# Kernel optimization log

Measured on AMD Instinct MI355X. Metric: run time of the kernel, lower is better.

The kernel has to match this reference:

```python
import jax, jax.numpy as jnp
import numpy as np

TEMP = 1.0

def setup_inputs() -> dict:
    key = jax.random.key(0)
    k1, k2, k3 = jax.random.split(key, 3)
    B, Lq, Lk, X, Dv = 16, 1024, 1024, 512, 512
    h_q = jax.random.normal(k1, (B, Lq, X), dtype=jnp.float32)
    h_k = jax.random.normal(k2, (B, Lk, X), dtype=jnp.float32)
    h_v = jax.random.normal(k3, (B, Lk, Dv), dtype=jnp.float32)
    return {"h_q": h_q, "h_k": h_k, "h_v": h_v}

def reference(h_q, h_k, h_v):
    # Original computes full cross-batch 'abx,cdx->acbd' then extracts the
    # batch diagonal; that equals a direct per-batch QK^T: [B,Lq,Lk].
    atten_score = jnp.einsum('bqx,bkx->bqk', h_q, h_k) / TEMP
    atten_prob = jax.nn.softmax(atten_score, axis=-1)  # dropout is identity in eval
    cxt = jnp.einsum('bqk,bkd->bqd', atten_prob, h_v)
    return cxt
```

## Files before the change

kernel.cpp:

```cpp
#include <hip/hip_runtime.h>

typedef _Float16 half8 __attribute__((ext_vector_type(8)));
typedef float f32x4 __attribute__((ext_vector_type(4)));
typedef unsigned short u16x8 __attribute__((ext_vector_type(8)));

#define LOG2E 1.44269504088896340736f

constexpr int NB = 16, LQ = 1024, LK = 1024, DX = 512, DVD = 512;
constexpr int QBLK = 64, KVB = 32, NCH = LK / KVB;
constexpr int TILE = KVB * DX;

static __device__ __forceinline__ unsigned short f2h(float f) {
  union { _Float16 h; unsigned short u; } c; c.h = (_Float16)f; return c.u;
}
static __device__ __forceinline__ unsigned int pack2(float a, float b) {
  union { _Float16 h[2]; unsigned int u; } c;
  c.h[0] = (_Float16)a; c.h[1] = (_Float16)b; return c.u;
}
static __device__ __forceinline__ void gload16(const unsigned short* g, unsigned short* l) {
  __builtin_amdgcn_global_load_lds(
      (const __attribute__((address_space(1))) unsigned int*)g,
      (__attribute__((address_space(3))) unsigned int*)l, 16, 0, 0);
}

__global__ __launch_bounds__(256) void prep_kv(
    const float* __restrict__ K, const float* __restrict__ V,
    unsigned short* __restrict__ Kw, unsigned short* __restrict__ Vw) {
  __shared__ float tile[32][520];
  const int bidx = blockIdx.x;
  const bool isV = bidx >= NB * NCH;
  const int bc = isV ? bidx - NB * NCH : bidx;
  const int t = (int)threadIdx.x;

  const float* src = (isV ? V : K) + (size_t)bc * (KVB * DX);
#pragma unroll
  for (int i = 0; i < 16; ++i) {
    int idx = t + i * 256;
    int r = idx >> 7, cc = (idx & 127) * 4;
    float4 v = *(const float4*)(src + (size_t)idx * 4);
    *(float4*)&tile[r][cc] = v;
  }
  __syncthreads();

  unsigned short* dst = (isV ? Vw : Kw) + (size_t)bc * TILE;
  if (!isV) {
#pragma unroll
    for (int k = 0; k < 8; ++k) {
      int obi = t * 8 + k;
      int p = obi >> 5, kv = obi & 31;
      const float* rp = &tile[kv][p * 8];
      u16x8 o = { f2h(rp[0]), f2h(rp[1]), f2h(rp[2]), f2h(rp[3]),
                  f2h(rp[4]), f2h(rp[5]), f2h(rp[6]), f2h(rp[7]) };
      *(u16x8*)(dst + obi * 8) = o;
    }
  } else {
#pragma unroll
    for (int k = 0; k < 8; ++k) {
      int vbi = t * 8 + k;
      int pv = vbi >> 9, d = vbi & 511;
      u16x8 o = { f2h(tile[pv * 8 + 0][d]), f2h(tile[pv * 8 + 1][d]),
                  f2h(tile[pv * 8 + 2][d]), f2h(tile[pv * 8 + 3][d]),
                  f2h(tile[pv * 8 + 4][d]), f2h(tile[pv * 8 + 5][d]),
                  f2h(tile[pv * 8 + 6][d]), f2h(tile[pv * 8 + 7][d]) };
      *(u16x8*)(dst + vbi * 8) = o;
    }
  }
}

__global__ __launch_bounds__(768) void attn_ws(
    const float* __restrict__ Qf, const unsigned short* __restrict__ Kw,
    const unsigned short* __restrict__ Vw, float* __restrict__ Out) {
  __shared__ __align__(16) unsigned short Kl[2][TILE];
  __shared__ __align__(16) unsigned short Vl[2][TILE];
  __shared__ __align__(16) unsigned short Pl[2][2048];
  __shared__ __align__(16) float sml[2][64];
  __shared__ __align__(16) float lfin[64];
  __shared__ __align__(16) int rflag[2][4];

  const int bid = blockIdx.x;
  const int logical = (bid & 7) * 32 + (bid >> 3);
  const int b  = logical >> 4;
  const int qt = logical & 15;
  const int tid = (int)threadIdx.x;
  const int lane = tid & 63;
  const int wave = tid >> 6;
  const bool isQK = wave < 4;
  const int qs = wave;
  const int wd = wave - 4;
  const int c15 = lane & 15;
  const int g4  = lane >> 4;
  const int rbase = g4 * 4;

  f32x4 blk[16];
  float mr = -3.0e38f, lr = 0.f;

  if (isQK) {
    const float* qrow = Qf + ((size_t)b * LQ + qt * QBLK + qs * 16 + c15) * DX + g4 * 8;
#pragma unroll
    for (int ks = 0; ks < 16; ++ks) {
      float4 a0 = *(const float4*)(qrow + ks * 32);
      float4 a1 = *(const float4*)(qrow + ks * 32 + 4);
      half8 f;
      f[0] = (_Float16)(a0.x * LOG2E); f[1] = (_Float16)(a0.y * LOG2E);
      f[2] = (_Float16)(a0.z * LOG2E); f[3] = (_Float16)(a0.w * LOG2E);
      f[4] = (_Float16)(a1.x * LOG2E); f[5] = (_Float16)(a1.y * LOG2E);
      f[6] = (_Float16)(a1.z * LOG2E); f[7] = (_Float16)(a1.w * LOG2E);
      blk[ks] = __builtin_bit_cast(f32x4, f);
    }
  } else {
#pragma unroll
    for (int i = 0; i < 16; ++i) blk[i] = (f32x4){0.f, 0.f, 0.f, 0.f};
  }

  const int st = tid - 256;
  const unsigned short* kg = Kw + (size_t)b * NCH * TILE + st * 8;
  const unsigned short* vg = Vw + (size_t)b * NCH * TILE + st * 8;

  if (tid >= 256) {
#pragma unroll
    for (int ii = 0; ii < 4; ++ii) gload16(kg + ii * 4096, &Kl[0][st * 8 + ii * 4096]);
  }
  __syncthreads();

  for (int p = 0; p <= NCH; ++p) {
    const int cb = p & 1, pbuf = cb ^ 1;

    if (tid >= 256) {
      if (p + 1 < NCH) {
        const unsigned short* ks_ = kg + (size_t)(p + 1) * TILE;
#pragma unroll
        for (int ii = 0; ii < 4; ++ii)
          gload16(ks_ + ii * 4096, &Kl[pbuf][st * 8 + ii * 4096]);
      }
      if (p < NCH) {
        const unsigned short* vs_ = vg + (size_t)p * TILE;
#pragma unroll
        for (int ii = 0; ii < 4; ++ii)
          gload16(vs_ + ii * 4096, &Vl[cb][st * 8 + ii * 4096]);
      }
    }

    if (isQK) {
      if (p < NCH) {
        f32x4 cs0 = {0.f, 0.f, 0.f, 0.f};
        f32x4 cs1 = {0.f, 0.f, 0.f, 0.f};
        __builtin_amdgcn_s_setprio(1);
#pragma unroll
        for (int ks = 0; ks < 16; ++ks) {
          const int po = (ks * 4 + g4) * 256;
          half8 a0 = *(const half8*)&Kl[cb][c15 * 8 + po];
          half8 a1 = *(const half8*)&Kl[cb][(16 + c15) * 8 + po];
          half8 qv = __builtin_bit_cast(half8, blk[ks]);
          cs0 = __builtin_amdgcn_mfma_f32_16x16x32_f16(a0, qv, cs0, 0, 0, 0);
          cs1 = __builtin_amdgcn_mfma_f32_16x16x32_f16(a1, qv, cs1, 0, 0, 0);
        }
        __builtin_amdgcn_s_setprio(0);

        float pm = fmaxf(fmaxf(fmaxf(cs0[0], cs0[1]), fmaxf(cs0[2], cs0[3])),
                         fmaxf(fmaxf(cs1[0], cs1[1]), fmaxf(cs1[2], cs1[3])));
        pm = fmaxf(pm, __shfl_xor(pm, 16, 64));
        pm = fmaxf(pm, __shfl_xor(pm, 32, 64));
        const bool resc = __any(pm > mr + 8.0f);
        float scl = 1.0f;
        if (resc) {
          float mn = fmaxf(mr, pm);
          scl = exp2f(mr - mn);
          mr = mn;
        }
        if (g4 == 0) sml[cb][qs * 16 + c15] = scl;
        if (lane == 0) rflag[cb][qs] = resc ? 1 : 0;
        float p0[4], p1[4];
#pragma unroll
        for (int j = 0; j < 4; ++j) {
          p0[j] = exp2f(cs0[j] - mr);
          p1[j] = exp2f(cs1[j] - mr);
        }
        float ps = ((p0[0] + p0[1]) + (p0[2] + p0[3]))
                 + ((p1[0] + p1[1]) + (p1[2] + p1[3]));
        ps += __shfl_xor(ps, 16, 64);
        ps += __shfl_xor(ps, 32, 64);
        lr = lr * scl + ps;

        {
          unsigned short* pw = &Pl[cb][(g4 >> 1) * 512 + (qs * 16 + c15) * 8 + (g4 & 1) * 4];
          uint2 w0 = { pack2(p0[0], p0[1]), pack2(p0[2], p0[3]) };
          uint2 w1 = { pack2(p1[0], p1[1]), pack2(p1[2], p1[3]) };
          *(uint2*)pw          = w0;
          *(uint2*)(pw + 1024) = w1;
        }
        if (p == NCH - 1 && g4 == 0) lfin[qs * 16 + c15] = lr;
      }
    } else {
      if (p > 0) {
        int4 f4 = *(const int4*)&rflag[pbuf][0];
        const int fl = f4.x | f4.y | f4.z | f4.w;
        half8 pa0 = *(const half8*)&Pl[pbuf][g4 * 512 + (c15) * 8];
        half8 pa1 = *(const half8*)&Pl[pbuf][g4 * 512 + (16 + c15) * 8];
        half8 pa2 = *(const half8*)&Pl[pbuf][g4 * 512 + (32 + c15) * 8];
        half8 pa3 = *(const half8*)&Pl[pbuf][g4 * 512 + (48 + c15) * 8];
        half8 bv0 = *(const half8*)&Vl[pbuf][g4 * 4096 + (wd * 64 + c15) * 8];
        half8 bv1 = *(const half8*)&Vl[pbuf][g4 * 4096 + (wd * 64 + 16 + c15) * 8];
        half8 bv2 = *(const half8*)&Vl[pbuf][g4 * 4096 + (wd * 64 + 32 + c15) * 8];
        half8 bv3 = *(const half8*)&Vl[pbuf][g4 * 4096 + (wd * 64 + 48 + c15) * 8];
        if (fl) {
#pragma unroll
          for (int s = 0; s < 4; ++s) {
            f32x4 sv = *(const f32x4*)&sml[pbuf][s * 16 + rbase];
#pragma unroll
            for (int n = 0; n < 4; ++n)
#pragma unroll
              for (int j = 0; j < 4; ++j) blk[s * 4 + n][j] *= sv[j];
          }
        }
        __builtin_amdgcn_s_setprio(1);
#pragma unroll
        for (int s = 0; s < 4; ++s) {
          half8 pas = (s == 0) ? pa0 : (s == 1) ? pa1 : (s == 2) ? pa2 : pa3;
          blk[s * 4 + 0] = __builtin_amdgcn_mfma_f32_16x16x32_f16(pas, bv0, blk[s * 4 + 0], 0, 0, 0);
          blk[s * 4 + 1] = __builtin_amdgcn_mfma_f32_16x16x32_f16(pas, bv1, blk[s * 4 + 1], 0, 0, 0);
          blk[s * 4 + 2] = __builtin_amdgcn_mfma_f32_16x16x32_f16(pas, bv2, blk[s * 4 + 2], 0, 0, 0);
          blk[s * 4 + 3] = __builtin_amdgcn_mfma_f32_16x16x32_f16(pas, bv3, blk[s * 4 + 3], 0, 0, 0);
        }
        __builtin_amdgcn_s_setprio(0);
      }
    }

    asm volatile("s_waitcnt vmcnt(0) lgkmcnt(0)" ::: "memory");
    __builtin_amdgcn_s_barrier();
    __builtin_amdgcn_sched_barrier(0);
  }

  if (!isQK) {
#pragma unroll
    for (int s = 0; s < 4; ++s) {
      f32x4 lv = *(const f32x4*)&lfin[s * 16 + rbase];
      float inv[4];
#pragma unroll
      for (int j = 0; j < 4; ++j) inv[j] = 1.0f / lv[j];
      float* ob = Out + ((size_t)b * LQ + qt * QBLK + s * 16 + rbase) * DVD
                  + wd * 64 + c15;
#pragma unroll
      for (int n = 0; n < 4; ++n)
#pragma unroll
        for (int j = 0; j < 4; ++j)
          ob[(size_t)j * DVD + n * 16] = blk[s * 4 + n][j] * inv[j];
    }
  }
}

extern "C" void kernel_launch(void* const* d_in, const int* in_sizes, int n_in,
                              void* d_out, int out_size, void* d_ws, size_t ws_size,
                              hipStream_t stream) {
  const float* Qf = (const float*)d_in[0];
  const float* Kf = (const float*)d_in[1];
  const float* Vf = (const float*)d_in[2];
  float* Out = (float*)d_out;

  unsigned short* Kw = (unsigned short*)d_ws;
  unsigned short* Vw = Kw + (size_t)NB * NCH * TILE;

  prep_kv<<<NB * NCH * 2, 256, 0, stream>>>(Kf, Vf, Kw, Vw);
  attn_ws<<<NB * (LQ / QBLK), 768, 0, stream>>>(Qf, Kw, Vw, Out);
}
```

Baseline: 79.96 us.

## Double KV chunk size and read V directly from global instead of LDS

Raises the KV chunk from 32 to 64 keys, halving the number of barrier-synchronised phases, and adjusts the prep kernel to emit the wider packed layout. V is no longer staged in LDS; the PV waves load their V fragments straight from global/L2 into registers. Only K is double-buffered in LDS, and the loader waves now also issue those copies. This frees LDS and cuts synchronisation, at the cost of exposing global-load latency on the V path, more register pressure, and a launch_bounds occupancy hint.

```diff
diff --git a/kernel.cpp b/kernel.cpp
--- a/kernel.cpp
+++ b/kernel.cpp
@@ -7,7 +7,7 @@
 #define LOG2E 1.44269504088896340736f
 
 constexpr int NB = 16, LQ = 1024, LK = 1024, DX = 512, DVD = 512;
-constexpr int QBLK = 64, KVB = 32, NCH = LK / KVB;
+constexpr int QBLK = 64, KVB = 64, NCH = LK / KVB;
 constexpr int TILE = KVB * DX;
 
 static __device__ __forceinline__ unsigned short f2h(float f) {
@@ -28,51 +28,51 @@
     unsigned short* __restrict__ Kw, unsigned short* __restrict__ Vw) {
   __shared__ float tile[32][520];
   const int bidx = blockIdx.x;
-  const bool isV = bidx >= NB * NCH;
-  const int bc = isV ? bidx - NB * NCH : bidx;
+  const bool isV = bidx >= NB * NCH * 2;
+  const int r = isV ? bidx - NB * NCH * 2 : bidx;
+  const int b = r >> 5, sub = r & 31, c = sub >> 1, half = sub & 1;
   const int t = (int)threadIdx.x;
 
-  const float* src = (isV ? V : K) + (size_t)bc * (KVB * DX);
+  const float* src = (isV ? V : K) + ((size_t)b * LK + c * 64 + half * 32) * DX;
 #pragma unroll
   for (int i = 0; i < 16; ++i) {
     int idx = t + i * 256;
-    int r = idx >> 7, cc = (idx & 127) * 4;
+    int rr = idx >> 7, cc = (idx & 127) * 4;
     float4 v = *(const float4*)(src + (size_t)idx * 4);
-    *(float4*)&tile[r][cc] = v;
+    *(float4*)&tile[rr][cc] = v;
   }
   __syncthreads();
 
-  unsigned short* dst = (isV ? Vw : Kw) + (size_t)bc * TILE;
+  unsigned short* dst = (isV ? Vw : Kw) + (size_t)(b * NCH + c) * TILE;
   if (!isV) {
 #pragma unroll
     for (int k = 0; k < 8; ++k) {
       int obi = t * 8 + k;
-      int p = obi >> 5, kv = obi & 31;
-      const float* rp = &tile[kv][p * 8];
+      int p = obi >> 5, kvloc = obi & 31;
+      const float* rp = &tile[kvloc][p * 8];
       u16x8 o = { f2h(rp[0]), f2h(rp[1]), f2h(rp[2]), f2h(rp[3]),
                   f2h(rp[4]), f2h(rp[5]), f2h(rp[6]), f2h(rp[7]) };
-      *(u16x8*)(dst + obi * 8) = o;
+      *(u16x8*)(dst + p * 512 + (half * 32 + kvloc) * 8) = o;
     }
   } else {
 #pragma unroll
     for (int k = 0; k < 8; ++k) {
       int vbi = t * 8 + k;
-      int pv = vbi >> 9, d = vbi & 511;
-      u16x8 o = { f2h(tile[pv * 8 + 0][d]), f2h(tile[pv * 8 + 1][d]),
-                  f2h(tile[pv * 8 + 2][d]), f2h(tile[pv * 8 + 3][d]),
-                  f2h(tile[pv * 8 + 4][d]), f2h(tile[pv * 8 + 5][d]),
-                  f2h(tile[pv * 8 + 6][d]), f2h(tile[pv * 8 + 7][d]) };
-      *(u16x8*)(dst + vbi * 8) = o;
-    }
-  }
-}
-
-__global__ __launch_bounds__(768) void attn_ws(
+      int pvloc = vbi >> 9, d = vbi & 511;
+      u16x8 o = { f2h(tile[pvloc * 8 + 0][d]), f2h(tile[pvloc * 8 + 1][d]),
+                  f2h(tile[pvloc * 8 + 2][d]), f2h(tile[pvloc * 8 + 3][d]),
+                  f2h(tile[pvloc * 8 + 4][d]), f2h(tile[pvloc * 8 + 5][d]),
+                  f2h(tile[pvloc * 8 + 6][d]), f2h(tile[pvloc * 8 + 7][d]) };
+      *(u16x8*)(dst + (half * 4 + pvloc) * 4096 + d * 8) = o;
+    }
+  }
+}
+
+__global__ __launch_bounds__(768, 3) void attn_ws2(
     const float* __restrict__ Qf, const unsigned short* __restrict__ Kw,
     const unsigned short* __restrict__ Vw, float* __restrict__ Out) {
   __shared__ __align__(16) unsigned short Kl[2][TILE];
-  __shared__ __align__(16) unsigned short Vl[2][TILE];
-  __shared__ __align__(16) unsigned short Pl[2][2048];
+  __shared__ __align__(16) unsigned short Pl[2][8 * 64 * 8];
   __shared__ __align__(16) float sml[2][64];
   __shared__ __align__(16) float lfin[64];
   __shared__ __align__(16) int rflag[2][4];
@@ -90,10 +90,11 @@
   const int c15 = lane & 15;
   const int g4  = lane >> 4;
   const int rbase = g4 * 4;
-
-  f32x4 blk[16];
+  const int d0 = wd * 64;
+
+  half8 qfrag[16];
+  f32x4 acc[16];
   float mr = -3.0e38f, lr = 0.f;
-
   if (isQK) {
     const float* qrow = Qf + ((size_t)b * LQ + qt * QBLK + qs * 16 + c15) * DX + g4 * 8;
 #pragma unroll
@@ -105,59 +106,52 @@
       f[2] = (_Float16)(a0.z * LOG2E); f[3] = (_Float16)(a0.w * LOG2E);
       f[4] = (_Float16)(a1.x * LOG2E); f[5] = (_Float16)(a1.y * LOG2E);
       f[6] = (_Float16)(a1.z * LOG2E); f[7] = (_Float16)(a1.w * LOG2E);
-      blk[ks] = __builtin_bit_cast(f32x4, f);
+      qfrag[ks] = f;
     }
   } else {
 #pragma unroll
-    for (int i = 0; i < 16; ++i) blk[i] = (f32x4){0.f, 0.f, 0.f, 0.f};
+    for (int i = 0; i < 16; ++i) acc[i] = (f32x4){0.f, 0.f, 0.f, 0.f};
   }
 
   const int st = tid - 256;
   const unsigned short* kg = Kw + (size_t)b * NCH * TILE + st * 8;
-  const unsigned short* vg = Vw + (size_t)b * NCH * TILE + st * 8;
+  const unsigned short* vgb = Vw + (size_t)b * NCH * TILE;
 
   if (tid >= 256) {
 #pragma unroll
-    for (int ii = 0; ii < 4; ++ii) gload16(kg + ii * 4096, &Kl[0][st * 8 + ii * 4096]);
+    for (int ii = 0; ii < 8; ++ii) gload16(kg + ii * 4096, &Kl[0][st * 8 + ii * 4096]);
   }
   __syncthreads();
 
-  for (int p = 0; p <= NCH; ++p) {
-    const int cb = p & 1, pbuf = cb ^ 1;
-
-    if (tid >= 256) {
-      if (p + 1 < NCH) {
-        const unsigned short* ks_ = kg + (size_t)(p + 1) * TILE;
-#pragma unroll
-        for (int ii = 0; ii < 4; ++ii)
-          gload16(ks_ + ii * 4096, &Kl[pbuf][st * 8 + ii * 4096]);
-      }
-      if (p < NCH) {
-        const unsigned short* vs_ = vg + (size_t)p * TILE;
-#pragma unroll
-        for (int ii = 0; ii < 4; ++ii)
-          gload16(vs_ + ii * 4096, &Vl[cb][st * 8 + ii * 4096]);
-      }
-    }
+  for (int ph = 0; ph <= NCH; ++ph) {
+    const int cb = ph & 1, pb = cb ^ 1;
 
     if (isQK) {
-      if (p < NCH) {
-        f32x4 cs0 = {0.f, 0.f, 0.f, 0.f};
-        f32x4 cs1 = {0.f, 0.f, 0.f, 0.f};
-        __builtin_amdgcn_s_setprio(1);
-#pragma unroll
-        for (int ks = 0; ks < 16; ++ks) {
-          const int po = (ks * 4 + g4) * 256;
-          half8 a0 = *(const half8*)&Kl[cb][c15 * 8 + po];
-          half8 a1 = *(const half8*)&Kl[cb][(16 + c15) * 8 + po];
-          half8 qv = __builtin_bit_cast(half8, blk[ks]);
-          cs0 = __builtin_amdgcn_mfma_f32_16x16x32_f16(a0, qv, cs0, 0, 0, 0);
-          cs1 = __builtin_amdgcn_mfma_f32_16x16x32_f16(a1, qv, cs1, 0, 0, 0);
-        }
-        __builtin_amdgcn_s_setprio(0);
+      if (ph < NCH) {
+        f32x4 cs0 = {0.f,0.f,0.f,0.f}, cs1 = {0.f,0.f,0.f,0.f};
+        f32x4 cs2 = {0.f,0.f,0.f,0.f}, cs3 = {0.f,0.f,0.f,0.f};
+        {
+          const unsigned short* kb = &Kl[cb][c15 * 8];
+          __builtin_amdgcn_s_setprio(1);
+#pragma unroll
+          for (int ks = 0; ks < 16; ++ks) {
+            const int po = (ks * 4 + g4) * 512;
+            half8 a0 = *(const half8*)(kb + po);
+            half8 a1 = *(const half8*)(kb + po + 128);
+            half8 a2 = *(const half8*)(kb + po + 256);
+            half8 a3 = *(const half8*)(kb + po + 384);
+            cs0 = __builtin_amdgcn_mfma_f32_16x16x32_f16(a0, qfrag[ks], cs0, 0, 0, 0);
+            cs1 = __builtin_amdgcn_mfma_f32_16x16x32_f16(a1, qfrag[ks], cs1, 0, 0, 0);
+            cs2 = __builtin_amdgcn_mfma_f32_16x16x32_f16(a2, qfrag[ks], cs2, 0, 0, 0);
+            cs3 = __builtin_amdgcn_mfma_f32_16x16x32_f16(a3, qfrag[ks], cs3, 0, 0, 0);
+          }
+          __builtin_amdgcn_s_setprio(0);
+        }
 
         float pm = fmaxf(fmaxf(fmaxf(cs0[0], cs0[1]), fmaxf(cs0[2], cs0[3])),
                          fmaxf(fmaxf(cs1[0], cs1[1]), fmaxf(cs1[2], cs1[3])));
+        pm = fmaxf(pm, fmaxf(fmaxf(fmaxf(cs2[0], cs2[1]), fmaxf(cs2[2], cs2[3])),
+                             fmaxf(fmaxf(cs3[0], cs3[1]), fmaxf(cs3[2], cs3[3]))));
         pm = fmaxf(pm, __shfl_xor(pm, 16, 64));
         pm = fmaxf(pm, __shfl_xor(pm, 32, 64));
         const bool resc = __any(pm > mr + 8.0f);
@@ -169,58 +163,76 @@
         }
         if (g4 == 0) sml[cb][qs * 16 + c15] = scl;
         if (lane == 0) rflag[cb][qs] = resc ? 1 : 0;
-        float p0[4], p1[4];
+
+        float p0[4], p1[4], p2[4], p3[4];
 #pragma unroll
         for (int j = 0; j < 4; ++j) {
           p0[j] = exp2f(cs0[j] - mr);
           p1[j] = exp2f(cs1[j] - mr);
-        }
-        float ps = ((p0[0] + p0[1]) + (p0[2] + p0[3]))
-                 + ((p1[0] + p1[1]) + (p1[2] + p1[3]));
-        ps += __shfl_xor(ps, 16, 64);
-        ps += __shfl_xor(ps, 32, 64);
-        lr = lr * scl + ps;
-
+          p2[j] = exp2f(cs2[j] - mr);
+          p3[j] = exp2f(cs3[j] - mr);
+        }
         {
           unsigned short* pw = &Pl[cb][(g4 >> 1) * 512 + (qs * 16 + c15) * 8 + (g4 & 1) * 4];
           uint2 w0 = { pack2(p0[0], p0[1]), pack2(p0[2], p0[3]) };
           uint2 w1 = { pack2(p1[0], p1[1]), pack2(p1[2], p1[3]) };
+          uint2 w2 = { pack2(p2[0], p2[1]), pack2(p2[2], p2[3]) };
+          uint2 w3 = { pack2(p3[0], p3[1]), pack2(p3[2], p3[3]) };
           *(uint2*)pw          = w0;
           *(uint2*)(pw + 1024) = w1;
-        }
-        if (p == NCH - 1 && g4 == 0) lfin[qs * 16 + c15] = lr;
+          *(uint2*)(pw + 2048) = w2;
+          *(uint2*)(pw + 3072) = w3;
+        }
+        float ps = ((p0[0] + p0[1]) + (p0[2] + p0[3])) + ((p1[0] + p1[1]) + (p1[2] + p1[3]))
+                 + ((p2[0] + p2[1]) + (p2[2] + p2[3])) + ((p3[0] + p3[1]) + (p3[2] + p3[3]));
+        ps += __shfl_xor(ps, 16, 64);
+        ps += __shfl_xor(ps, 32, 64);
+        lr = lr * scl + ps;
+        if (ph == NCH - 1 && g4 == 0) lfin[qs * 16 + c15] = lr;
       }
     } else {
-      if (p > 0) {
-        int4 f4 = *(const int4*)&rflag[pbuf][0];
+      half8 bv[2][4];
+      if (ph > 0) {
+        const unsigned short* vt = vgb + (size_t)(ph - 1) * TILE;
+#pragma unroll
+        for (int t = 0; t < 2; ++t)
+#pragma unroll
+          for (int n = 0; n < 4; ++n)
+            bv[t][n] = *(const half8*)(vt + (t * 4 + g4) * 4096 + (d0 + n * 16 + c15) * 8);
+      }
+      if (ph + 1 < NCH) {
+        const unsigned short* ks_ = kg + (size_t)(ph + 1) * TILE;
+#pragma unroll
+        for (int ii = 0; ii < 8; ++ii)
+          gload16(ks_ + ii * 4096, &Kl[pb][st * 8 + ii * 4096]);
+      }
+      if (ph > 0) {
+        half8 pa[4][2];
+#pragma unroll
+        for (int s = 0; s < 4; ++s)
+#pragma unroll
+          for (int t = 0; t < 2; ++t)
+            pa[s][t] = *(const half8*)&Pl[pb][(t * 4 + g4) * 512 + (s * 16 + c15) * 8];
+        int4 f4 = *(const int4*)&rflag[pb][0];
         const int fl = f4.x | f4.y | f4.z | f4.w;
-        half8 pa0 = *(const half8*)&Pl[pbuf][g4 * 512 + (c15) * 8];
-        half8 pa1 = *(const half8*)&Pl[pbuf][g4 * 512 + (16 + c15) * 8];
-        half8 pa2 = *(const half8*)&Pl[pbuf][g4 * 512 + (32 + c15) * 8];
-        half8 pa3 = *(const half8*)&Pl[pbuf][g4 * 512 + (48 + c15) * 8];
-        half8 bv0 = *(const half8*)&Vl[pbuf][g4 * 4096 + (wd * 64 + c15) * 8];
-        half8 bv1 = *(const half8*)&Vl[pbuf][g4 * 4096 + (wd * 64 + 16 + c15) * 8];
-        half8 bv2 = *(const half8*)&Vl[pbuf][g4 * 4096 + (wd * 64 + 32 + c15) * 8];
-        half8 bv3 = *(const half8*)&Vl[pbuf][g4 * 4096 + (wd * 64 + 48 + c15) * 8];
         if (fl) {
 #pragma unroll
           for (int s = 0; s < 4; ++s) {
-            f32x4 sv = *(const f32x4*)&sml[pbuf][s * 16 + rbase];
+            f32x4 sv = *(const f32x4*)&sml[pb][s * 16 + rbase];
 #pragma unroll
             for (int n = 0; n < 4; ++n)
 #pragma unroll
-              for (int j = 0; j < 4; ++j) blk[s * 4 + n][j] *= sv[j];
+              for (int j = 0; j < 4; ++j) acc[s * 4 + n][j] *= sv[j];
           }
         }
         __builtin_amdgcn_s_setprio(1);
 #pragma unroll
-        for (int s = 0; s < 4; ++s) {
-          half8 pas = (s == 0) ? pa0 : (s == 1) ? pa1 : (s == 2) ? pa2 : pa3;
-          blk[s * 4 + 0] = __builtin_amdgcn_mfma_f32_16x16x32_f16(pas, bv0, blk[s * 4 + 0], 0, 0, 0);
-          blk[s * 4 + 1] = __builtin_amdgcn_mfma_f32_16x16x32_f16(pas, bv1, blk[s * 4 + 1], 0, 0, 0);
-          blk[s * 4 + 2] = __builtin_amdgcn_mfma_f32_16x16x32_f16(pas, bv2, blk[s * 4 + 2], 0, 0, 0);
-          blk[s * 4 + 3] = __builtin_amdgcn_mfma_f32_16x16x32_f16(pas, bv3, blk[s * 4 + 3], 0, 0, 0);
-        }
+        for (int s = 0; s < 4; ++s)
+#pragma unroll
+          for (int n = 0; n < 4; ++n) {
+            acc[s * 4 + n] = __builtin_amdgcn_mfma_f32_16x16x32_f16(pa[s][0], bv[0][n], acc[s * 4 + n], 0, 0, 0);
+            acc[s * 4 + n] = __builtin_amdgcn_mfma_f32_16x16x32_f16(pa[s][1], bv[1][n], acc[s * 4 + n], 0, 0, 0);
+          }
         __builtin_amdgcn_s_setprio(0);
       }
     }
@@ -237,13 +249,12 @@
       float inv[4];
 #pragma unroll
       for (int j = 0; j < 4; ++j) inv[j] = 1.0f / lv[j];
-      float* ob = Out + ((size_t)b * LQ + qt * QBLK + s * 16 + rbase) * DVD
-                  + wd * 64 + c15;
+      float* ob = Out + ((size_t)b * LQ + qt * QBLK + s * 16 + rbase) * DVD + d0 + c15;
 #pragma unroll
       for (int n = 0; n < 4; ++n)
 #pragma unroll
         for (int j = 0; j < 4; ++j)
-          ob[(size_t)j * DVD + n * 16] = blk[s * 4 + n][j] * inv[j];
+          ob[(size_t)j * DVD + n * 16] = acc[s * 4 + n][j] * inv[j];
     }
   }
 }
@@ -259,6 +270,6 @@
   unsigned short* Kw = (unsigned short*)d_ws;
   unsigned short* Vw = Kw + (size_t)NB * NCH * TILE;
 
-  prep_kv<<<NB * NCH * 2, 256, 0, stream>>>(Kf, Vf, Kw, Vw);
-  attn_ws<<<NB * (LQ / QBLK), 768, 0, stream>>>(Qf, Kw, Vw, Out);
-}
+  prep_kv<<<NB * NCH * 2 * 2, 256, 0, stream>>>(Kf, Vf, Kw, Vw);
+  attn_ws2<<<NB * (LQ / QBLK), 768, 0, stream>>>(Qf, Kw, Vw, Out);
+}
```

Result: slower. 121.5 us (+51.9%).

## Halve query block and LDS footprint with single-buffered K/V tiles

Applied to the files above, without the earlier changes.

Shrinks the query block from 64 to 32 rows, so there are twice as many workgroups, each with 2 QK waves and 4 PV waves that each own 128 output columns. K and V are now single-buffered in LDS, and loads for the next chunk are issued after the barrier instead of double-buffered ahead. This cuts LDS use per block so more blocks can be resident per CU and the grid fills the device better. The cost is that each K/V tile is read from memory twice as often, and prefetch now overlaps less with compute, which may expose load latency.

```diff
diff --git a/kernel.cpp b/kernel.cpp
--- a/kernel.cpp
+++ b/kernel.cpp
@@ -7,7 +7,7 @@
 #define LOG2E 1.44269504088896340736f
 
 constexpr int NB = 16, LQ = 1024, LK = 1024, DX = 512, DVD = 512;
-constexpr int QBLK = 64, KVB = 32, NCH = LK / KVB;
+constexpr int QBLK = 32, KVB = 32, NCH = LK / KVB;
 constexpr int TILE = KVB * DX;
 
 static __device__ __forceinline__ unsigned short f2h(float f) {
@@ -67,29 +67,30 @@
   }
 }
 
-__global__ __launch_bounds__(768) void attn_ws(
+__global__ __launch_bounds__(384) void attn_db(
     const float* __restrict__ Qf, const unsigned short* __restrict__ Kw,
     const unsigned short* __restrict__ Vw, float* __restrict__ Out) {
-  __shared__ __align__(16) unsigned short Kl[2][TILE];
-  __shared__ __align__(16) unsigned short Vl[2][TILE];
-  __shared__ __align__(16) unsigned short Pl[2][2048];
-  __shared__ __align__(16) float sml[2][64];
-  __shared__ __align__(16) float lfin[64];
-  __shared__ __align__(16) int rflag[2][4];
+  __shared__ __align__(16) unsigned short Kl[TILE];
+  __shared__ __align__(16) unsigned short Vl[TILE];
+  __shared__ __align__(16) unsigned short Pl[2][1024];
+  __shared__ __align__(16) float sml[2][32];
+  __shared__ __align__(16) float lfin[32];
+  __shared__ __align__(16) int rflag[2][2];
 
   const int bid = blockIdx.x;
-  const int logical = (bid & 7) * 32 + (bid >> 3);
-  const int b  = logical >> 4;
-  const int qt = logical & 15;
+  const int logical = (bid & 7) * 64 + (bid >> 3);
+  const int b  = logical >> 5;
+  const int qt = logical & 31;
   const int tid = (int)threadIdx.x;
   const int lane = tid & 63;
   const int wave = tid >> 6;
-  const bool isQK = wave < 4;
+  const bool isQK = wave < 2;
   const int qs = wave;
-  const int wd = wave - 4;
+  const int wd = wave - 2;
   const int c15 = lane & 15;
   const int g4  = lane >> 4;
   const int rbase = g4 * 4;
+  const int d0 = wd * 128;
 
   f32x4 blk[16];
   float mr = -3.0e38f, lr = 0.f;
@@ -112,49 +113,38 @@
     for (int i = 0; i < 16; ++i) blk[i] = (f32x4){0.f, 0.f, 0.f, 0.f};
   }
 
-  const int st = tid - 256;
+  const int st = tid - 128;
   const unsigned short* kg = Kw + (size_t)b * NCH * TILE + st * 8;
   const unsigned short* vg = Vw + (size_t)b * NCH * TILE + st * 8;
 
-  if (tid >= 256) {
-#pragma unroll
-    for (int ii = 0; ii < 4; ++ii) gload16(kg + ii * 4096, &Kl[0][st * 8 + ii * 4096]);
-  }
+  if (!isQK) {
+#pragma unroll
+    for (int ii = 0; ii < 8; ++ii) gload16(kg + ii * 2048, &Kl[st * 8 + ii * 2048]);
+  }
+  asm volatile("s_waitcnt vmcnt(0)" ::: "memory");
   __syncthreads();
 
-  for (int p = 0; p <= NCH; ++p) {
-    const int cb = p & 1, pbuf = cb ^ 1;
-
-    if (tid >= 256) {
-      if (p + 1 < NCH) {
-        const unsigned short* ks_ = kg + (size_t)(p + 1) * TILE;
-#pragma unroll
-        for (int ii = 0; ii < 4; ++ii)
-          gload16(ks_ + ii * 4096, &Kl[pbuf][st * 8 + ii * 4096]);
-      }
-      if (p < NCH) {
-        const unsigned short* vs_ = vg + (size_t)p * TILE;
-#pragma unroll
-        for (int ii = 0; ii < 4; ++ii)
-          gload16(vs_ + ii * 4096, &Vl[cb][st * 8 + ii * 4096]);
-      }
-    }
+  for (int ph = 0; ph <= NCH; ++ph) {
+    const int cb = ph & 1, pb = cb ^ 1;
 
     if (isQK) {
-      if (p < NCH) {
+      if (ph < NCH) {
         f32x4 cs0 = {0.f, 0.f, 0.f, 0.f};
         f32x4 cs1 = {0.f, 0.f, 0.f, 0.f};
-        __builtin_amdgcn_s_setprio(1);
-#pragma unroll
-        for (int ks = 0; ks < 16; ++ks) {
-          const int po = (ks * 4 + g4) * 256;
-          half8 a0 = *(const half8*)&Kl[cb][c15 * 8 + po];
-          half8 a1 = *(const half8*)&Kl[cb][(16 + c15) * 8 + po];
-          half8 qv = __builtin_bit_cast(half8, blk[ks]);
-          cs0 = __builtin_amdgcn_mfma_f32_16x16x32_f16(a0, qv, cs0, 0, 0, 0);
-          cs1 = __builtin_amdgcn_mfma_f32_16x16x32_f16(a1, qv, cs1, 0, 0, 0);
-        }
-        __builtin_amdgcn_s_setprio(0);
+        {
+          const unsigned short* kb = &Kl[c15 * 8 + g4 * 256];
+          __builtin_amdgcn_s_setprio(1);
+#pragma unroll
+          for (int ks = 0; ks < 16; ++ks) {
+            const unsigned short* kp = kb + ks * 1024;
+            half8 a0 = *(const half8*)kp;
+            half8 a1 = *(const half8*)(kp + 128);
+            half8 qv = __builtin_bit_cast(half8, blk[ks]);
+            cs0 = __builtin_amdgcn_mfma_f32_16x16x32_f16(a0, qv, cs0, 0, 0, 0);
+            cs1 = __builtin_amdgcn_mfma_f32_16x16x32_f16(a1, qv, cs1, 0, 0, 0);
+          }
+          __builtin_amdgcn_s_setprio(0);
+        }
 
         float pm = fmaxf(fmaxf(fmaxf(cs0[0], cs0[1]), fmaxf(cs0[2], cs0[3])),
                          fmaxf(fmaxf(cs1[0], cs1[1]), fmaxf(cs1[2], cs1[3])));
@@ -182,46 +172,58 @@
         lr = lr * scl + ps;
 
         {
-          unsigned short* pw = &Pl[cb][(g4 >> 1) * 512 + (qs * 16 + c15) * 8 + (g4 & 1) * 4];
+          unsigned short* pw = &Pl[cb][(g4 >> 1) * 256 + (qs * 16 + c15) * 8 + (g4 & 1) * 4];
           uint2 w0 = { pack2(p0[0], p0[1]), pack2(p0[2], p0[3]) };
           uint2 w1 = { pack2(p1[0], p1[1]), pack2(p1[2], p1[3]) };
-          *(uint2*)pw          = w0;
-          *(uint2*)(pw + 1024) = w1;
-        }
-        if (p == NCH - 1 && g4 == 0) lfin[qs * 16 + c15] = lr;
+          *(uint2*)pw         = w0;
+          *(uint2*)(pw + 512) = w1;
+        }
+        if (ph == NCH - 1 && g4 == 0) lfin[qs * 16 + c15] = lr;
       }
     } else {
-      if (p > 0) {
-        int4 f4 = *(const int4*)&rflag[pbuf][0];
-        const int fl = f4.x | f4.y | f4.z | f4.w;
-        half8 pa0 = *(const half8*)&Pl[pbuf][g4 * 512 + (c15) * 8];
-        half8 pa1 = *(const half8*)&Pl[pbuf][g4 * 512 + (16 + c15) * 8];
-        half8 pa2 = *(const half8*)&Pl[pbuf][g4 * 512 + (32 + c15) * 8];
-        half8 pa3 = *(const half8*)&Pl[pbuf][g4 * 512 + (48 + c15) * 8];
-        half8 bv0 = *(const half8*)&Vl[pbuf][g4 * 4096 + (wd * 64 + c15) * 8];
-        half8 bv1 = *(const half8*)&Vl[pbuf][g4 * 4096 + (wd * 64 + 16 + c15) * 8];
-        half8 bv2 = *(const half8*)&Vl[pbuf][g4 * 4096 + (wd * 64 + 32 + c15) * 8];
-        half8 bv3 = *(const half8*)&Vl[pbuf][g4 * 4096 + (wd * 64 + 48 + c15) * 8];
+      if (ph > 0) {
+        half8 pa0 = *(const half8*)&Pl[pb][g4 * 256 + c15 * 8];
+        half8 pa1 = *(const half8*)&Pl[pb][g4 * 256 + (16 + c15) * 8];
+        half8 bv[8];
+#pragma unroll
+        for (int n = 0; n < 8; ++n)
+          bv[n] = *(const half8*)&Vl[g4 * 4096 + (d0 + n * 16 + c15) * 8];
+        const int fl = rflag[pb][0] | rflag[pb][1];
         if (fl) {
-#pragma unroll
-          for (int s = 0; s < 4; ++s) {
-            f32x4 sv = *(const f32x4*)&sml[pbuf][s * 16 + rbase];
-#pragma unroll
-            for (int n = 0; n < 4; ++n)
-#pragma unroll
-              for (int j = 0; j < 4; ++j) blk[s * 4 + n][j] *= sv[j];
-          }
+          f32x4 sv0 = *(const f32x4*)&sml[pb][rbase];
+          f32x4 sv1 = *(const f32x4*)&sml[pb][16 + rbase];
+#pragma unroll
+          for (int n = 0; n < 8; ++n)
+#pragma unroll
+            for (int j = 0; j < 4; ++j) {
+              blk[n][j]     *= sv0[j];
+              blk[8 + n][j] *= sv1[j];
+            }
         }
         __builtin_amdgcn_s_setprio(1);
 #pragma unroll
-        for (int s = 0; s < 4; ++s) {
-          half8 pas = (s == 0) ? pa0 : (s == 1) ? pa1 : (s == 2) ? pa2 : pa3;
-          blk[s * 4 + 0] = __builtin_amdgcn_mfma_f32_16x16x32_f16(pas, bv0, blk[s * 4 + 0], 0, 0, 0);
-          blk[s * 4 + 1] = __builtin_amdgcn_mfma_f32_16x16x32_f16(pas, bv1, blk[s * 4 + 1], 0, 0, 0);
-          blk[s * 4 + 2] = __builtin_amdgcn_mfma_f32_16x16x32_f16(pas, bv2, blk[s * 4 + 2], 0, 0, 0);
-          blk[s * 4 + 3] = __builtin_amdgcn_mfma_f32_16x16x32_f16(pas, bv3, blk[s * 4 + 3], 0, 0, 0);
+        for (int n = 0; n < 8; ++n) {
+          blk[n]     = __builtin_amdgcn_mfma_f32_16x16x32_f16(pa0, bv[n], blk[n], 0, 0, 0);
+          blk[8 + n] = __builtin_amdgcn_mfma_f32_16x16x32_f16(pa1, bv[n], blk[8 + n], 0, 0, 0);
         }
         __builtin_amdgcn_s_setprio(0);
+      }
+    }
+
+    asm volatile("s_waitcnt lgkmcnt(0)" ::: "memory");
+    __builtin_amdgcn_s_barrier();
+    __builtin_amdgcn_sched_barrier(0);
+
+    if (!isQK) {
+      if (ph + 1 < NCH) {
+        const unsigned short* ks_ = kg + (size_t)(ph + 1) * TILE;
+#pragma unroll
+        for (int ii = 0; ii < 8; ++ii) gload16(ks_ + ii * 2048, &Kl[st * 8 + ii * 2048]);
+      }
+      if (ph < NCH) {
+        const unsigned short* vs_ = vg + (size_t)ph * TILE;
+#pragma unroll
+        for (int ii = 0; ii < 8; ++ii) gload16(vs_ + ii * 2048, &Vl[st * 8 + ii * 2048]);
       }
     }
 
@@ -232,18 +234,17 @@
 
   if (!isQK) {
 #pragma unroll
-    for (int s = 0; s < 4; ++s) {
+    for (int s = 0; s < 2; ++s) {
       f32x4 lv = *(const f32x4*)&lfin[s * 16 + rbase];
       float inv[4];
 #pragma unroll
       for (int j = 0; j < 4; ++j) inv[j] = 1.0f / lv[j];
-      float* ob = Out + ((size_t)b * LQ + qt * QBLK + s * 16 + rbase) * DVD
-                  + wd * 64 + c15;
-#pragma unroll
-      for (int n = 0; n < 4; ++n)
+      float* ob = Out + ((size_t)b * LQ + qt * QBLK + s * 16 + rbase) * DVD + d0 + c15;
+#pragma unroll
+      for (int n = 0; n < 8; ++n)
 #pragma unroll
         for (int j = 0; j < 4; ++j)
-          ob[(size_t)j * DVD + n * 16] = blk[s * 4 + n][j] * inv[j];
+          ob[(size_t)j * DVD + n * 16] = blk[s * 8 + n][j] * inv[j];
     }
   }
 }
@@ -260,5 +261,5 @@
   unsigned short* Vw = Kw + (size_t)NB * NCH * TILE;
 
   prep_kv<<<NB * NCH * 2, 256, 0, stream>>>(Kf, Vf, Kw, Vw);
-  attn_ws<<<NB * (LQ / QBLK), 768, 0, stream>>>(Qf, Kw, Vw, Out);
-}
+  attn_db<<<NB * (LQ / QBLK), 384, 0, stream>>>(Qf, Kw, Vw, Out);
+}
```

After: 159.1 us. +99.0%, slower.
